# Optimization experiments

Measured on AMD Instinct MI355X. Metric: run time of the kernel, lower is better.

## Reference

```python
import jax, jax.numpy as jnp
import numpy as np


def _binarize_ste(t):
    # torch code overwrites .data with sign(), which acts as a straight-through
    # identity for autograd: forward = sign(t), backward = identity.
    return t + jax.lax.stop_gradient(jnp.sign(t) - t)


def setup_inputs() -> dict:
    key = jax.random.key(0)
    k1, k2 = jax.random.split(key)
    B, C_IN, C_OUT = 512, 1536, 512
    x = jax.random.normal(k1, (B, C_IN), dtype=jnp.float32)
    stdv = 1.0 / np.sqrt(C_OUT * C_IN)
    weight = jax.random.uniform(k2, (C_OUT, C_IN), dtype=jnp.float32,
                                minval=-stdv, maxval=stdv)
    return {"x": x, "weight": weight}


def reference(x, weight):
    B, c_in = x.shape
    c_out = weight.shape[0]
    G = c_in // 3  # majority-3 group count
    bx = _binarize_ste(x)        # [B, c_in] in {-1, 0, +1}
    bw = _binarize_ste(weight)   # [c_out, c_in]
    # einsum('bj,cj->bcj') then group-sum over triples == contract only within
    # each group of 3, never materializing the full [B, c_out, c_in] tensor.
    inter = jnp.einsum('bgk,cgk->bcg',
                       bx.reshape(B, G, 3),
                       bw.reshape(c_out, G, 3))  # [B, c_out, G]
    out = 2.25 * jnp.sum(jnp.clip(inter, -1.0, 1.0), axis=-1)  # [B, c_out]
    return out
```

## Files before the change

kernel.cpp:

```cpp
#include <hip/hip_runtime.h>
#include <stdint.h>


#define CIN     1536
#define B_DIM   512
#define COUT    512
#define GROUPS  512
#define ROW_U4  24
#define XSTRIDE 25

__global__ __launch_bounds__(256) void pack_kernel(
    const float* __restrict__ x, const float* __restrict__ w,
    uint32_t* __restrict__ packed) {
  const int gw   = blockIdx.x * 4 + (threadIdx.x >> 6);
  const int lane = threadIdx.x & 63;
  const int row  = gw >> 1;
  const int half = gw & 1;
  const float* src = (row < B_DIM) ? (x + (size_t)row * CIN)
                                   : (w + (size_t)(row - B_DIM) * CIN);
  const int j = lane >> 1;
  const int hi = lane & 1;

  #pragma unroll
  for (int si = 0; si < 4; si++) {
    const int s = 4 * half + si;
    const float3 f = ((const float3*)src)[64 * s + lane];
    unsigned long long P0 = __ballot(f.x > 0.0f);
    unsigned long long N0 = __ballot(f.x < 0.0f);
    unsigned long long P1 = __ballot(f.y > 0.0f);
    unsigned long long N1 = __ballot(f.y < 0.0f);
    unsigned long long P2 = __ballot(f.z > 0.0f);
    unsigned long long N2 = __ballot(f.z < 0.0f);
    unsigned h0 = hi ? (unsigned)(P0 >> 32) : (unsigned)P0;
    unsigned h1 = hi ? (unsigned)(P1 >> 32) : (unsigned)P1;
    unsigned h2 = hi ? (unsigned)(P2 >> 32) : (unsigned)P2;
    unsigned h3 = hi ? (unsigned)(N0 >> 32) : (unsigned)N0;
    unsigned h4 = hi ? (unsigned)(N1 >> 32) : (unsigned)N1;
    unsigned h5 = hi ? (unsigned)(N2 >> 32) : (unsigned)N2;
    unsigned v01 = (j == 1) ? h1 : h0;
    unsigned v23 = (j == 3) ? h3 : h2;
    unsigned v45 = (j == 5) ? h5 : h4;
    unsigned val = (j < 2) ? v01 : ((j < 4) ? v23 : v45);
    if (lane < 12) packed[(size_t)row * 96 + s * 12 + lane] = val;
  }
}

__device__ __forceinline__ void maj32(
    unsigned xp0, unsigned xp1, unsigned xp2,
    unsigned xn0, unsigned xn1, unsigned xn2,
    unsigned wp0, unsigned wp1, unsigned wp2,
    unsigned wn0, unsigned wn1, unsigned wn2,
    int& acc) {
  unsigned pos0 = (xp0 & wp0) | (xn0 & wn0);
  unsigned pos1 = (xp1 & wp1) | (xn1 & wn1);
  unsigned pos2 = (xp2 & wp2) | (xn2 & wn2);
  unsigned neg0 = (xp0 & wn0) | (xn0 & wp0);
  unsigned neg1 = (xp1 & wn1) | (xn1 & wp1);
  unsigned neg2 = (xp2 & wn2) | (xn2 & wp2);
  unsigned sa  = pos0 ^ pos1;
  unsigned cp0 = sa ^ pos2;
  unsigned cp1 = (pos0 & pos1) | (pos2 & sa);
  unsigned sb  = neg0 ^ neg1;
  unsigned cn0 = sb ^ neg2;
  unsigned cn1 = (neg0 & neg1) | (neg2 & sb);
  unsigned nh = ~cn1;
  unsigned nl = ~cn0;
  unsigned hi = cp1 & nh;
  unsigned eq = ~(cp1 ^ cn1);
  unsigned gt = hi | (eq & (cp0 & nl));
  unsigned ge = hi | (eq & (cp0 | nl));
  acc += __popc(gt) + __popc(ge);
}

__global__ __launch_bounds__(256, 8) void maj3_kernel(
    const uint4* __restrict__ px, const uint4* __restrict__ pw,
    float* __restrict__ out) {
  __shared__ __align__(16) uint4 sx[16][XSTRIDE];
  __shared__ __align__(16) uint4 sw[8][XSTRIDE];
  __shared__ int comb[128];

  const int b0 = blockIdx.y * 16;
  const int c0 = blockIdx.x * 8;
  const int tid = threadIdx.x;

  const uint4* gx = px + (size_t)b0 * ROW_U4;
  const uint4* gw = pw + (size_t)c0 * ROW_U4;
  #pragma unroll
  for (int i = tid; i < 16 * ROW_U4; i += 256) {
    int r = i / ROW_U4, wd = i - r * ROW_U4;
    sx[r][wd] = gx[i];
  }
  if (tid < 8 * ROW_U4) {
    int r = tid / ROW_U4, wd = tid - r * ROW_U4;
    sw[r][wd] = gw[tid];
  }
  __syncthreads();

  const int o  = tid & 127;
  const int tx = o & 7;
  const int ty = o >> 3;
  const int h  = tid >> 7;

  const uint4* xr = &sx[ty][h * 12];
  const uint4* wr = &sw[tx][h * 12];

  int acc = 0;
  #pragma unroll
  for (int i = 0; i < 4; i++) {
    uint4 a0 = xr[3 * i], a1 = xr[3 * i + 1], a2 = xr[3 * i + 2];
    uint4 b0v = wr[3 * i], b1 = wr[3 * i + 1], b2 = wr[3 * i + 2];
    maj32(a0.x, a0.z, a1.x, a1.z, a2.x, a2.z,
          b0v.x, b0v.z, b1.x, b1.z, b2.x, b2.z, acc);
    maj32(a0.y, a0.w, a1.y, a1.w, a2.y, a2.w,
          b0v.y, b0v.w, b1.y, b1.w, b2.y, b2.w, acc);
  }

  if (h == 1) comb[o] = acc;
  __syncthreads();
  if (h == 0) {
    int total = acc + comb[o];
    out[(size_t)(b0 + ty) * COUT + (c0 + tx)] = 2.25f * (float)(total - GROUPS);
  }
}

extern "C" void kernel_launch(void* const* d_in, const int* in_sizes, int n_in,
                              void* d_out, int out_size, void* d_ws, size_t ws_size,
                              hipStream_t stream) {
  const float* x = (const float*)d_in[0];
  const float* w = (const float*)d_in[1];
  float* out = (float*)d_out;

  uint32_t* packed = (uint32_t*)d_ws;
  const uint4* px = (const uint4*)packed;
  const uint4* pw = (const uint4*)(packed + (size_t)B_DIM * 96);

  pack_kernel<<<512, 256, 0, stream>>>(x, w, packed);

  dim3 grid(COUT / 8, B_DIM / 16);
  maj3_kernel<<<grid, 256, 0, stream>>>(px, pw, out);
}
```

Baseline: 64.63 us.

## Use 16x16 output tiles with 2x2 register blocking and 4-way K split

Each block now computes a 16x16 output tile instead of 16x8, halving the grid. Each thread computes a 2x2 micro-tile over a quarter of the reduction, so every x and w chunk loaded from shared memory is reused twice. Partial sums are combined through a 4x256 shared buffer. The shared-memory load is simplified to one fixed three-uint4 copy per thread. The change cuts LDS traffic and block count, but leaves fewer blocks to fill the GPU and adds more register pressure.

```diff
diff --git a/kernel.cpp b/kernel.cpp
--- a/kernel.cpp
+++ b/kernel.cpp
@@ -72,55 +72,70 @@
   acc += __popc(gt) + __popc(ge);
 }
 
-__global__ __launch_bounds__(256, 8) void maj3_kernel(
+__device__ __forceinline__ void chunk_bc(
+    const uint4& a0, const uint4& a1, const uint4& a2,
+    const uint4& b0, const uint4& b1, const uint4& b2,
+    int& acc) {
+  maj32(a0.x, a0.z, a1.x, a1.z, a2.x, a2.z,
+        b0.x, b0.z, b1.x, b1.z, b2.x, b2.z, acc);
+  maj32(a0.y, a0.w, a1.y, a1.w, a2.y, a2.w,
+        b0.y, b0.w, b1.y, b1.w, b2.y, b2.w, acc);
+}
+
+__global__ __launch_bounds__(256, 4) void maj3_kernel(
     const uint4* __restrict__ px, const uint4* __restrict__ pw,
     float* __restrict__ out) {
   __shared__ __align__(16) uint4 sx[16][XSTRIDE];
-  __shared__ __align__(16) uint4 sw[8][XSTRIDE];
-  __shared__ int comb[128];
+  __shared__ __align__(16) uint4 sw[16][XSTRIDE];
+  __shared__ int comb[4][256];
 
   const int b0 = blockIdx.y * 16;
-  const int c0 = blockIdx.x * 8;
+  const int c0 = blockIdx.x * 16;
   const int tid = threadIdx.x;
 
-  const uint4* gx = px + (size_t)b0 * ROW_U4;
-  const uint4* gw = pw + (size_t)c0 * ROW_U4;
-  #pragma unroll
-  for (int i = tid; i < 16 * ROW_U4; i += 256) {
-    int r = i / ROW_U4, wd = i - r * ROW_U4;
-    sx[r][wd] = gx[i];
-  }
-  if (tid < 8 * ROW_U4) {
-    int r = tid / ROW_U4, wd = tid - r * ROW_U4;
-    sw[r][wd] = gw[tid];
+  {
+    const int r  = tid >> 3;
+    const int wd = (tid & 7) * 3;
+    const uint4* g = (r < 16) ? (px + (size_t)(b0 + r) * ROW_U4 + wd)
+                              : (pw + (size_t)(c0 + r - 16) * ROW_U4 + wd);
+    uint4* d = (r < 16) ? &sx[r][wd] : &sw[r - 16][wd];
+    d[0] = g[0]; d[1] = g[1]; d[2] = g[2];
   }
   __syncthreads();
 
-  const int o  = tid & 127;
-  const int tx = o & 7;
-  const int ty = o >> 3;
-  const int h  = tid >> 7;
+  const int t2c = tid & 7;
+  const int t2b = (tid >> 3) & 7;
+  const int q   = tid >> 6;
 
-  const uint4* xr = &sx[ty][h * 12];
-  const uint4* wr = &sw[tx][h * 12];
+  const uint4* xr0 = &sx[2 * t2b][q * 6];
+  const uint4* xr1 = &sx[2 * t2b + 1][q * 6];
+  const uint4* wc0 = &sw[2 * t2c][q * 6];
+  const uint4* wc1 = &sw[2 * t2c + 1][q * 6];
 
-  int acc = 0;
+  int a00 = 0, a01 = 0, a10 = 0, a11 = 0;
   #pragma unroll
-  for (int i = 0; i < 4; i++) {
-    uint4 a0 = xr[3 * i], a1 = xr[3 * i + 1], a2 = xr[3 * i + 2];
-    uint4 b0v = wr[3 * i], b1 = wr[3 * i + 1], b2 = wr[3 * i + 2];
-    maj32(a0.x, a0.z, a1.x, a1.z, a2.x, a2.z,
-          b0v.x, b0v.z, b1.x, b1.z, b2.x, b2.z, acc);
-    maj32(a0.y, a0.w, a1.y, a1.w, a2.y, a2.w,
-          b0v.y, b0v.w, b1.y, b1.w, b2.y, b2.w, acc);
+  for (int i = 0; i < 2; i++) {
+    uint4 xa0 = xr0[3 * i], xa1 = xr0[3 * i + 1], xa2 = xr0[3 * i + 2];
+    uint4 xb0 = xr1[3 * i], xb1 = xr1[3 * i + 1], xb2 = xr1[3 * i + 2];
+    uint4 wa0 = wc0[3 * i], wa1 = wc0[3 * i + 1], wa2 = wc0[3 * i + 2];
+    uint4 wb0 = wc1[3 * i], wb1 = wc1[3 * i + 1], wb2 = wc1[3 * i + 2];
+    chunk_bc(xa0, xa1, xa2, wa0, wa1, wa2, a00);
+    chunk_bc(xa0, xa1, xa2, wb0, wb1, wb2, a01);
+    chunk_bc(xb0, xb1, xb2, wa0, wa1, wa2, a10);
+    chunk_bc(xb0, xb1, xb2, wb0, wb1, wb2, a11);
   }
 
-  if (h == 1) comb[o] = acc;
+  const int ob = 2 * t2b, oc = 2 * t2c;
+  comb[q][ob * 16 + oc]           = a00;
+  comb[q][ob * 16 + oc + 1]       = a01;
+  comb[q][(ob + 1) * 16 + oc]     = a10;
+  comb[q][(ob + 1) * 16 + oc + 1] = a11;
   __syncthreads();
-  if (h == 0) {
-    int total = acc + comb[o];
-    out[(size_t)(b0 + ty) * COUT + (c0 + tx)] = 2.25f * (float)(total - GROUPS);
-  }
+
+  const int o = tid;
+  int total = comb[0][o] + comb[1][o] + comb[2][o] + comb[3][o];
+  out[(size_t)(b0 + (o >> 4)) * COUT + c0 + (o & 15)] =
+      2.25f * (float)(total - GROUPS);
 }
 
 extern "C" void kernel_launch(void* const* d_in, const int* in_sizes, int n_in,
@@ -136,6 +151,6 @@
 
   pack_kernel<<<512, 256, 0, stream>>>(x, w, packed);
 
-  dim3 grid(COUT / 8, B_DIM / 16);
+  dim3 grid(COUT / 16, B_DIM / 16);
   maj3_kernel<<<grid, 256, 0, stream>>>(px, pw, out);
 }
```

Result: no change. 63.98 us, median of 2 (-1.0%).
